# Performance work log

Hardware: AMD Instinct MI355X
Metric: run time of the kernel (lower is better)

## Reference

```python
import jax, jax.numpy as jnp
import numpy as np

N_NODES = 100000
N_EDGES = 1000000
NUM_FEATURES = 64
HIDDEN = 64
NUM_GRAPHS = 128


def setup_inputs() -> dict:
    key = jax.random.key(0)
    ks = jax.random.split(key, 12)
    x = jax.random.normal(ks[0], (N_NODES, NUM_FEATURES), dtype=jnp.float32)
    edge_index = jax.random.randint(ks[1], (2, N_EDGES), 0, N_NODES, dtype=jnp.int64)
    edge_weight = jax.random.uniform(ks[2], (N_EDGES,), dtype=jnp.float32)
    batch = jnp.sort(jax.random.randint(ks[3], (N_NODES,), 0, NUM_GRAPHS, dtype=jnp.int64))
    s1 = 1.0 / np.sqrt(NUM_FEATURES)
    s2 = 1.0 / np.sqrt(HIDDEN)
    # GraphConv layer 1: lin_rel (with bias) applied to aggregated msgs, lin_root (no bias)
    w1_rel = jax.random.uniform(ks[4], (HIDDEN, NUM_FEATURES), jnp.float32, -s1, s1)
    b1_rel = jax.random.uniform(ks[5], (HIDDEN,), jnp.float32, -s1, s1)
    w1_root = jax.random.uniform(ks[6], (HIDDEN, NUM_FEATURES), jnp.float32, -s1, s1)
    # GraphConv layer 2
    w2_rel = jax.random.uniform(ks[7], (HIDDEN, HIDDEN), jnp.float32, -s2, s2)
    b2_rel = jax.random.uniform(ks[8], (HIDDEN,), jnp.float32, -s2, s2)
    w2_root = jax.random.uniform(ks[9], (HIDDEN, HIDDEN), jnp.float32, -s2, s2)
    # final Linear(hidden, 1)
    w_lin = jax.random.uniform(ks[10], (1, HIDDEN), jnp.float32, -s2, s2)
    b_lin = jax.random.uniform(ks[11], (1,), jnp.float32, -s2, s2)
    return {
        "x": x, "edge_index": edge_index, "edge_weight": edge_weight, "batch": batch,
        "w1_rel": w1_rel, "b1_rel": b1_rel, "w1_root": w1_root,
        "w2_rel": w2_rel, "b2_rel": b2_rel, "w2_root": w2_root,
        "w_lin": w_lin, "b_lin": b_lin,
    }


def graph_conv(x, edge_index, edge_weight, w_rel, b_rel, w_root):
    # messages: x[src] * e, scatter-add into dst  (gather-scale-scatter)
    src, dst = edge_index[0], edge_index[1]
    msgs = x[src] * edge_weight[:, None]                      # [E, F]
    aggr = jax.ops.segment_sum(msgs, dst, num_segments=x.shape[0])  # [N, F]
    return aggr @ w_rel.T + b_rel + x @ w_root.T


def reference(x, edge_index, edge_weight, batch,
              w1_rel, b1_rel, w1_root, w2_rel, b2_rel, w2_root, w_lin, b_lin):
    h = graph_conv(x, edge_index, edge_weight, w1_rel, b1_rel, w1_root)
    h = jax.nn.relu(h)
    h = graph_conv(h, edge_index, edge_weight, w2_rel, b2_rel, w2_root)
    # global_mean_pool over graph ids
    sums = jax.ops.segment_sum(h, batch, num_segments=NUM_GRAPHS)          # [G, H]
    counts = jax.ops.segment_sum(jnp.ones((h.shape[0],), h.dtype), batch,
                                 num_segments=NUM_GRAPHS)                  # [G]
    pooled = sums / jnp.maximum(counts, 1.0)[:, None]
    # dropout(p=0.5) in eval mode is identity
    return pooled @ w_lin.T + b_lin                                        # [G, 1]
```

## Files before the change

kernel.cpp:

```cpp
#include <hip/hip_runtime.h>
#include <hip/hip_bf16.h>


#define N_NODES 100000
#define N_EDGES 1000000
#define NGRAPHS 128
#define BN 512
#define NBUCK ((N_NODES + BN - 1) / BN)
#define FILL_T 16
#define FILL_TILE (256 * FILL_T)
#define FILL_NB ((N_EDGES + FILL_TILE - 1) / FILL_TILE)

typedef __attribute__((ext_vector_type(8))) short bf16x8;
typedef __attribute__((ext_vector_type(8))) unsigned short u16x8;
typedef __attribute__((ext_vector_type(4))) float f32x4;

__device__ __forceinline__ unsigned short f2bf(float f) {
    unsigned u = __float_as_uint(f);
    unsigned r = (u + 0x7FFFu + ((u >> 16) & 1u)) >> 16;
    return (unsigned short)r;
}
__device__ __forceinline__ float bf2f(unsigned short h) {
    return __uint_as_float(((unsigned)h) << 16);
}

__global__ __launch_bounds__(256) void prep_cvt_kernel(
    const float* __restrict__ x, unsigned short* __restrict__ xh, int n8,
    const float* __restrict__ w1rel, const float* __restrict__ w1root,
    const float* __restrict__ w2rel, const float* __restrict__ w2root,
    const float* __restrict__ wlin, const float* __restrict__ b2rel,
    const float* __restrict__ blin, unsigned short* __restrict__ whirel,
    unsigned short* __restrict__ wlorel, unsigned short* __restrict__ whiroot,
    unsigned short* __restrict__ wloroot, float* __restrict__ u,
    float* __restrict__ v, float* __restrict__ C) {
    int tid = threadIdx.x;
    int i = blockIdx.x * 256 + tid;
    if (i < n8) {
        const float4* xp = (const float4*)x + (size_t)i * 2;
        float4 a = xp[0], b = xp[1];
        u16x8 o;
        o[0] = f2bf(a.x); o[1] = f2bf(a.y); o[2] = f2bf(a.z); o[3] = f2bf(a.w);
        o[4] = f2bf(b.x); o[5] = f2bf(b.y); o[6] = f2bf(b.z); o[7] = f2bf(b.w);
        *((u16x8*)xh + i) = o;
        return;
    }
    for (int k = tid; k < 4096; k += 256) {
        float a = w1rel[k];
        unsigned short hi = f2bf(a);
        whirel[k] = hi;
        wlorel[k] = f2bf(a - bf2f(hi));
        float b = w1root[k];
        unsigned short hb = f2bf(b);
        whiroot[k] = hb;
        wloroot[k] = f2bf(b - bf2f(hb));
    }
    if (tid < 64) {
        float uu = 0.f, vv = 0.f;
        for (int h = 0; h < 64; ++h) {
            float wl = wlin[h];
            uu += wl * w2rel[h * 64 + tid];
            vv += wl * w2root[h * 64 + tid];
        }
        u[tid] = uu;
        v[tid] = vv;
    }
    if (tid == 0) {
        float c = blin[0];
        for (int h = 0; h < 64; ++h) c += wlin[h] * b2rel[h];
        *C = c;
    }
}

__global__ __launch_bounds__(256) void bucket_hist(const int* __restrict__ ei,
                                                   int* __restrict__ bcount,
                                                   int E) {
    __shared__ int lh[NBUCK];
    int tid = threadIdx.x;
    for (int i = tid; i < NBUCK; i += 256) lh[i] = 0;
    __syncthreads();
    for (int e = blockIdx.x * 256 + tid; e < E; e += gridDim.x * 256)
        atomicAdd(&lh[ei[E + e] >> 9], 1);
    __syncthreads();
    for (int i = tid; i < NBUCK; i += 256) {
        int c = lh[i];
        if (c) atomicAdd(&bcount[i], c);
    }
}

__global__ void bucket_scan(const int* __restrict__ bcount,
                            int* __restrict__ boff, int* __restrict__ cursor) {
    __shared__ int s[256];
    int t = threadIdx.x;
    int v = (t < NBUCK) ? bcount[t] : 0;
    s[t] = v;
    __syncthreads();
    for (int off = 1; off < 256; off <<= 1) {
        int x = (t >= off) ? s[t - off] : 0;
        __syncthreads();
        s[t] += x;
        __syncthreads();
    }
    if (t < NBUCK) {
        boff[t] = s[t] - v;
        cursor[t] = s[t] - v;
    }
    if (t == 255) boff[NBUCK] = s[255];
}

__global__ __launch_bounds__(256) void bucket_fill(
    const int* __restrict__ ei, const float* __restrict__ ew,
    int* __restrict__ cursor, int2* __restrict__ ebuf, int E) {
    __shared__ int lh[NBUCK];
    __shared__ int gbase[NBUCK];
    int tid = threadIdx.x;
    for (int i = tid; i < NBUCK; i += 256) lh[i] = 0;
    __syncthreads();
    int base = blockIdx.x * FILL_TILE;
    int2 rec[FILL_T];
    int meta[FILL_T];
#pragma unroll
    for (int i = 0; i < FILL_T; ++i) {
        int e = base + i * 256 + tid;
        meta[i] = -1;
        if (e < E) {
            int src = ei[e];
            int dst = ei[E + e];
            int b = dst >> 9;
            int r = atomicAdd(&lh[b], 1);
            rec[i].x = src | ((dst & (BN - 1)) << 17);
            rec[i].y = __float_as_int(ew[e]);
            meta[i] = (b << 13) | r;
        }
    }
    __syncthreads();
    for (int i = tid; i < NBUCK; i += 256) {
        int c = lh[i];
        gbase[i] = c ? atomicAdd(&cursor[i], c) : 0;
    }
    __syncthreads();
#pragma unroll
    for (int i = 0; i < FILL_T; ++i) {
        if (meta[i] >= 0) {
            int b = meta[i] >> 13;
            int r = meta[i] & 8191;
            ebuf[gbase[b] + r] = rec[i];
        }
    }
}

__global__ __launch_bounds__(512) void csr_build(
    const int* __restrict__ boff, const int2* __restrict__ ebuf,
    const int* __restrict__ batch, int* __restrict__ row_ptr,
    int2* __restrict__ csr, int N) {
    __shared__ int s[BN];
    int b = blockIdx.x;
    int t = threadIdx.x;
    int beg = boff[b], end = boff[b + 1];
    s[t] = 0;
    __syncthreads();
    for (int j = beg + t; j < end; j += 512)
        atomicAdd(&s[(ebuf[j].x >> 17) & (BN - 1)], 1);
    __syncthreads();
    int v = s[t];
    for (int off = 1; off < BN; off <<= 1) {
        int x = (t >= off) ? s[t - off] : 0;
        __syncthreads();
        s[t] += x;
        __syncthreads();
    }
    int excl = s[t] - v;
    int gidx = b * BN + t;
    if (gidx <= N) row_ptr[gidx] = beg + excl;
    __syncthreads();
    s[t] = excl;
    __syncthreads();
    for (int j = beg + t; j < end; j += 512) {
        int2 rec = ebuf[j];
        int dlo = (rec.x >> 17) & (BN - 1);
        int g = batch[b * BN + dlo];
        int r = atomicAdd(&s[dlo], 1);
        int2 o;
        o.x = (rec.x & 0x1FFFF) | (g << 17);
        o.y = rec.y;
        csr[beg + r] = o;
    }
}

__global__ __launch_bounds__(256) void gather_kernel(
    const unsigned short* __restrict__ xh, const int* __restrict__ row_ptr,
    const int2* __restrict__ csr, unsigned short* __restrict__ aggr, int N,
    int chunk) {
    int lane = threadIdx.x & 63;
    int wid = (blockIdx.x * blockDim.x + threadIdx.x) >> 6;
    int g = lane >> 4;
    int c = lane & 15;
    int n0 = wid * chunk;
    int n1 = min(n0 + chunk, N);
    for (int node = n0; node < n1; ++node) {
        int beg = row_ptr[node], end = row_ptr[node + 1];
        float4 acc = {0.f, 0.f, 0.f, 0.f};
        for (int j0 = beg; j0 < end; j0 += 64) {
            int cnt = min(64, end - j0);
            int2 e = {0, 0};
            if (lane < cnt) e = csr[j0 + lane];
            for (int k = 0; k < cnt; k += 4) {
                int myk = k + g;
                int sj = __shfl(e.x, myk) & 0x1FFFF;
                float wj = __int_as_float(__shfl(e.y, myk));
                if (myk < cnt) {
                    ushort4 xv =
                        *(const ushort4*)(xh + (size_t)sj * 64 + c * 4);
                    acc.x += wj * bf2f(xv.x);
                    acc.y += wj * bf2f(xv.y);
                    acc.z += wj * bf2f(xv.z);
                    acc.w += wj * bf2f(xv.w);
                }
            }
        }
#pragma unroll
        for (int off = 16; off < 64; off <<= 1) {
            acc.x += __shfl_xor(acc.x, off);
            acc.y += __shfl_xor(acc.y, off);
            acc.z += __shfl_xor(acc.z, off);
            acc.w += __shfl_xor(acc.w, off);
        }
        if (lane < 16) {
            ushort4 o;
            o.x = f2bf(acc.x);
            o.y = f2bf(acc.y);
            o.z = f2bf(acc.z);
            o.w = f2bf(acc.w);
            *(ushort4*)(aggr + (size_t)node * 64 + c * 4) = o;
        }
    }
}

__global__ __launch_bounds__(256, 2) void dense_kernel(
    const unsigned short* __restrict__ aggr,
    const unsigned short* __restrict__ xh,
    const unsigned short* __restrict__ whirel,
    const unsigned short* __restrict__ wlorel,
    const unsigned short* __restrict__ whiroot,
    const unsigned short* __restrict__ wloroot,
    const float* __restrict__ b1rel, const float* __restrict__ u,
    const float* __restrict__ v, float* __restrict__ p, float* __restrict__ q,
    int N) {
    int lane = threadIdx.x & 63;
    int wave = (blockIdx.x << 2) + (threadIdx.x >> 6);
    int nb = wave * 16;
    if (nb >= N) return;
    int lo4 = lane & 15;
    int quad = lane >> 4;

    f32x4 acc[4];
#pragma unroll
    for (int t = 0; t < 4; ++t) acc[t] = (f32x4){0.f, 0.f, 0.f, 0.f};

    for (int s = 0; s < 2; ++s) {
        bf16x8 Aa = *(const bf16x8*)(aggr + (size_t)(nb + lo4) * 64 + s * 32 +
                                     quad * 8);
        bf16x8 Ax = *(const bf16x8*)(xh + (size_t)(nb + lo4) * 64 + s * 32 +
                                     quad * 8);
#pragma unroll
        for (int t = 0; t < 4; ++t) {
            int off = (t * 16 + lo4) * 64 + s * 32 + quad * 8;
            bf16x8 bhr = *(const bf16x8*)(whirel + off);
            bf16x8 blr = *(const bf16x8*)(wlorel + off);
            bf16x8 bhx = *(const bf16x8*)(whiroot + off);
            bf16x8 blx = *(const bf16x8*)(wloroot + off);
            acc[t] = __builtin_amdgcn_mfma_f32_16x16x32_bf16(Aa, bhr, acc[t],
                                                             0, 0, 0);
            acc[t] = __builtin_amdgcn_mfma_f32_16x16x32_bf16(Aa, blr, acc[t],
                                                             0, 0, 0);
            acc[t] = __builtin_amdgcn_mfma_f32_16x16x32_bf16(Ax, bhx, acc[t],
                                                             0, 0, 0);
            acc[t] = __builtin_amdgcn_mfma_f32_16x16x32_bf16(Ax, blx, acc[t],
                                                             0, 0, 0);
        }
    }

    float pc[4] = {0.f, 0.f, 0.f, 0.f};
    float qc[4] = {0.f, 0.f, 0.f, 0.f};
#pragma unroll
    for (int t = 0; t < 4; ++t) {
        float bb = b1rel[t * 16 + lo4];
        float uu = u[t * 16 + lo4];
        float vv = v[t * 16 + lo4];
#pragma unroll
        for (int r = 0; r < 4; ++r) {
            float h1 = fmaxf(acc[t][r] + bb, 0.f);
            pc[r] += uu * h1;
            qc[r] += vv * h1;
        }
    }
#pragma unroll
    for (int off = 1; off < 16; off <<= 1) {
#pragma unroll
        for (int r = 0; r < 4; ++r) {
            pc[r] += __shfl_xor(pc[r], off);
            qc[r] += __shfl_xor(qc[r], off);
        }
    }
    if (lo4 == 0) {
        f32x4 po = {pc[0], pc[1], pc[2], pc[3]};
        f32x4 qo = {qc[0], qc[1], qc[2], qc[3]};
        *(f32x4*)(p + nb + quad * 4) = po;
        *(f32x4*)(q + nb + quad * 4) = qo;
    }
}

#define PT_EPT 4
#define PT_EPW (64 * PT_EPT)
#define PT_NB ((N_EDGES + 4 * PT_EPW - 1) / (4 * PT_EPW))
#define PS_NB 98
__global__ __launch_bounds__(256) void pool_both(
    const int2* __restrict__ csr, const float* __restrict__ p,
    const float* __restrict__ q, const int* __restrict__ batch,
    float* __restrict__ gp, float* __restrict__ gq, float* __restrict__ gc,
    int E, int N) {
    __shared__ float lbuf[2 * NGRAPHS];
    int tid = threadIdx.x;
    lbuf[tid] = 0.f;
    __syncthreads();
    if (blockIdx.x < PT_NB) {
        int lane = tid & 63;
        int wid = (blockIdx.x * 256 + tid) >> 6;
        int base = wid * PT_EPW;
        float acc = 0.f;
        int curg = -1;
#pragma unroll
        for (int i = 0; i < PT_EPT; ++i) {
            int j = base + i * 64 + lane;
            if (j < E) {
                int2 e = csr[j];
                int g = (e.x >> 17) & 127;
                float val = __int_as_float(e.y) * p[e.x & 0x1FFFF];
                if (g != curg) {
                    if (curg >= 0) atomicAdd(&lbuf[curg], acc);
                    curg = g;
                    acc = 0.f;
                }
                acc += val;
            }
        }
        if (curg >= 0) atomicAdd(&lbuf[curg], acc);
        __syncthreads();
        if (tid < NGRAPHS) {
            float t = lbuf[tid];
            if (t != 0.f) atomicAdd(&gp[tid], t);
        }
    } else {
        int bid = blockIdx.x - PT_NB;
        for (int i = bid * 256 + tid; i < N; i += PS_NB * 256) {
            int g = batch[i];
            atomicAdd(&lbuf[g], q[i]);
            atomicAdd(&lbuf[NGRAPHS + g], 1.f);
        }
        __syncthreads();
        if (tid < NGRAPHS) {
            if (lbuf[NGRAPHS + tid] != 0.f) {
                atomicAdd(&gq[tid], lbuf[tid]);
                atomicAdd(&gc[tid], lbuf[NGRAPHS + tid]);
            }
        }
    }
}

__global__ void final_kernel(const float* __restrict__ gp,
                             const float* __restrict__ gq,
                             const float* __restrict__ gc,
                             const float* __restrict__ C,
                             float* __restrict__ out) {
    int g = threadIdx.x;
    float c = fmaxf(gc[g], 1.0f);
    out[g] = (gp[g] + gq[g]) / c + *C;
}

extern "C" void kernel_launch(void* const* d_in, const int* in_sizes, int n_in,
                              void* d_out, int out_size, void* d_ws,
                              size_t ws_size, hipStream_t stream) {
    const float* x      = (const float*)d_in[0];
    const int*   ei     = (const int*)d_in[1];
    const float* ew     = (const float*)d_in[2];
    const int*   batch  = (const int*)d_in[3];
    const float* w1rel  = (const float*)d_in[4];
    const float* b1rel  = (const float*)d_in[5];
    const float* w1root = (const float*)d_in[6];
    const float* w2rel  = (const float*)d_in[7];
    const float* b2rel  = (const float*)d_in[8];
    const float* w2root = (const float*)d_in[9];
    const float* wlin   = (const float*)d_in[10];
    const float* blin   = (const float*)d_in[11];
    float* out = (float*)d_out;

    char* wsb = (char*)d_ws;
    int2* csr  = (int2*)wsb;
    unsigned short* aggr = (unsigned short*)(wsb + (size_t)N_EDGES * 8);
    int2* ebuf = (int2*)aggr;
    char* tail = wsb + (size_t)N_EDGES * 8 + (size_t)N_NODES * 128;
    unsigned short* whirel  = (unsigned short*)tail;
    unsigned short* wlorel  = whirel + 4096;
    unsigned short* whiroot = wlorel + 4096;
    unsigned short* wloroot = whiroot + 4096;
    float* p  = (float*)(wloroot + 4096);
    float* q  = p + N_NODES;
    float* u  = q + N_NODES;
    float* v  = u + 64;
    float* C  = v + 64;
    int*   bcount = (int*)(C + 1);
    float* gp = (float*)(bcount + NBUCK);
    float* gq = gp + NGRAPHS;
    float* gc = gq + NGRAPHS;
    int*   boff   = (int*)(gc + NGRAPHS);
    int*   cursor = boff + (NBUCK + 1);
    int*   row_ptr = cursor + NBUCK;
    unsigned short* xh = (unsigned short*)(row_ptr + N_NODES + 2);

    hipMemsetAsync(bcount, 0, (NBUCK + 3 * NGRAPHS) * sizeof(int), stream);

    int n8 = N_NODES * 64 / 8;
    prep_cvt_kernel<<<n8 / 256 + 1, 256, 0, stream>>>(
        x, xh, n8, w1rel, w1root, w2rel, w2root, wlin, b2rel, blin, whirel,
        wlorel, whiroot, wloroot, u, v, C);

    bucket_hist<<<256, 256, 0, stream>>>(ei, bcount, N_EDGES);
    bucket_scan<<<1, 256, 0, stream>>>(bcount, boff, cursor);
    bucket_fill<<<FILL_NB, 256, 0, stream>>>(ei, ew, cursor, ebuf, N_EDGES);
    csr_build<<<NBUCK, 512, 0, stream>>>(boff, ebuf, batch, row_ptr, csr,
                                         N_NODES);

    {
        int blocks = 2048;
        int waves = blocks * 4;
        int chunk = (N_NODES + waves - 1) / waves;
        gather_kernel<<<blocks, 256, 0, stream>>>(xh, row_ptr, csr, aggr,
                                                  N_NODES, chunk);
    }
    {
        int tiles = N_NODES / 16;
        int blocks = (tiles + 3) / 4;
        dense_kernel<<<blocks, 256, 0, stream>>>(aggr, xh, whirel, wlorel,
                                                 whiroot, wloroot, b1rel, u, v,
                                                 p, q, N_NODES);
    }
    pool_both<<<PT_NB + PS_NB, 256, 0, stream>>>(csr, p, q, batch, gp, gq, gc,
                                                 N_EDGES, N_NODES);
    final_kernel<<<1, NGRAPHS, 0, stream>>>(gp, gq, gc, C, out);
}
```

Baseline: 229.7 us.

## Fuse bf16 conversion with bucket histogram; widen gather loads to 16 bytes

Merges the x-to-bf16 conversion, weight prep and edge-destination histogram into one launch, using block-index ranges so the independent jobs run side by side and one kernel launch is saved. The gather kernel now has each lane load 8 bf16 values (16 bytes) instead of 4, so 8 edges are in flight per step rather than 4 and each step issues fewer, wider memory requests. It also doubles the edges handled per thread in the pooling kernel. The risks are more registers per lane in gather, an extra shuffle-reduction stage, and the histogram blocks now competing with the conversion blocks for the GPU at the same time.

```diff
diff --git a/kernel.cpp b/kernel.cpp
--- a/kernel.cpp
+++ b/kernel.cpp
@@ -10,6 +10,8 @@
 #define FILL_T 16
 #define FILL_TILE (256 * FILL_T)
 #define FILL_NB ((N_EDGES + FILL_TILE - 1) / FILL_TILE)
+#define CVT_NB (N_NODES * 64 / 8 / 256)
+#define HIST_NB 256
 
 typedef __attribute__((ext_vector_type(8))) short bf16x8;
 typedef __attribute__((ext_vector_type(8))) unsigned short u16x8;
@@ -24,8 +26,9 @@
     return __uint_as_float(((unsigned)h) << 16);
 }
 
-__global__ __launch_bounds__(256) void prep_cvt_kernel(
-    const float* __restrict__ x, unsigned short* __restrict__ xh, int n8,
+__global__ __launch_bounds__(256) void prep_cvt_hist_kernel(
+    const float* __restrict__ x, unsigned short* __restrict__ xh,
+    const int* __restrict__ ei, int* __restrict__ bcount,
     const float* __restrict__ w1rel, const float* __restrict__ w1root,
     const float* __restrict__ w2rel, const float* __restrict__ w2root,
     const float* __restrict__ wlin, const float* __restrict__ b2rel,
@@ -34,52 +37,51 @@
     unsigned short* __restrict__ wloroot, float* __restrict__ u,
     float* __restrict__ v, float* __restrict__ C) {
     int tid = threadIdx.x;
-    int i = blockIdx.x * 256 + tid;
-    if (i < n8) {
+    int b = blockIdx.x;
+    if (b < CVT_NB) {
+        int i = b * 256 + tid;
         const float4* xp = (const float4*)x + (size_t)i * 2;
-        float4 a = xp[0], b = xp[1];
+        float4 a = xp[0], bb = xp[1];
         u16x8 o;
         o[0] = f2bf(a.x); o[1] = f2bf(a.y); o[2] = f2bf(a.z); o[3] = f2bf(a.w);
-        o[4] = f2bf(b.x); o[5] = f2bf(b.y); o[6] = f2bf(b.z); o[7] = f2bf(b.w);
+        o[4] = f2bf(bb.x); o[5] = f2bf(bb.y); o[6] = f2bf(bb.z); o[7] = f2bf(bb.w);
         *((u16x8*)xh + i) = o;
         return;
     }
-    for (int k = tid; k < 4096; k += 256) {
-        float a = w1rel[k];
-        unsigned short hi = f2bf(a);
-        whirel[k] = hi;
-        wlorel[k] = f2bf(a - bf2f(hi));
-        float b = w1root[k];
-        unsigned short hb = f2bf(b);
-        whiroot[k] = hb;
-        wloroot[k] = f2bf(b - bf2f(hb));
-    }
-    if (tid < 64) {
-        float uu = 0.f, vv = 0.f;
-        for (int h = 0; h < 64; ++h) {
-            float wl = wlin[h];
-            uu += wl * w2rel[h * 64 + tid];
-            vv += wl * w2root[h * 64 + tid];
-        }
-        u[tid] = uu;
-        v[tid] = vv;
-    }
-    if (tid == 0) {
-        float c = blin[0];
-        for (int h = 0; h < 64; ++h) c += wlin[h] * b2rel[h];
-        *C = c;
-    }
-}
-
-__global__ __launch_bounds__(256) void bucket_hist(const int* __restrict__ ei,
-                                                   int* __restrict__ bcount,
-                                                   int E) {
+    if (b == CVT_NB) {
+        for (int k = tid; k < 4096; k += 256) {
+            float a = w1rel[k];
+            unsigned short hi = f2bf(a);
+            whirel[k] = hi;
+            wlorel[k] = f2bf(a - bf2f(hi));
+            float w = w1root[k];
+            unsigned short hb = f2bf(w);
+            whiroot[k] = hb;
+            wloroot[k] = f2bf(w - bf2f(hb));
+        }
+        if (tid < 64) {
+            float uu = 0.f, vv = 0.f;
+            for (int h = 0; h < 64; ++h) {
+                float wl = wlin[h];
+                uu += wl * w2rel[h * 64 + tid];
+                vv += wl * w2root[h * 64 + tid];
+            }
+            u[tid] = uu;
+            v[tid] = vv;
+        }
+        if (tid == 0) {
+            float c = blin[0];
+            for (int h = 0; h < 64; ++h) c += wlin[h] * b2rel[h];
+            *C = c;
+        }
+        return;
+    }
     __shared__ int lh[NBUCK];
-    int tid = threadIdx.x;
+    int hb = b - CVT_NB - 1;
     for (int i = tid; i < NBUCK; i += 256) lh[i] = 0;
     __syncthreads();
-    for (int e = blockIdx.x * 256 + tid; e < E; e += gridDim.x * 256)
-        atomicAdd(&lh[ei[E + e] >> 9], 1);
+    for (int e = hb * 256 + tid; e < N_EDGES; e += HIST_NB * 256)
+        atomicAdd(&lh[ei[N_EDGES + e] >> 9], 1);
     __syncthreads();
     for (int i = tid; i < NBUCK; i += 256) {
         int c = lh[i];
@@ -192,45 +194,40 @@
     int chunk) {
     int lane = threadIdx.x & 63;
     int wid = (blockIdx.x * blockDim.x + threadIdx.x) >> 6;
-    int g = lane >> 4;
-    int c = lane & 15;
+    int g = lane >> 3;
+    int c = lane & 7;
     int n0 = wid * chunk;
     int n1 = min(n0 + chunk, N);
     for (int node = n0; node < n1; ++node) {
         int beg = row_ptr[node], end = row_ptr[node + 1];
-        float4 acc = {0.f, 0.f, 0.f, 0.f};
+        float acc[8];
+#pragma unroll
+        for (int t = 0; t < 8; ++t) acc[t] = 0.f;
         for (int j0 = beg; j0 < end; j0 += 64) {
             int cnt = min(64, end - j0);
             int2 e = {0, 0};
             if (lane < cnt) e = csr[j0 + lane];
-            for (int k = 0; k < cnt; k += 4) {
+            for (int k = 0; k < cnt; k += 8) {
                 int myk = k + g;
                 int sj = __shfl(e.x, myk) & 0x1FFFF;
                 float wj = __int_as_float(__shfl(e.y, myk));
                 if (myk < cnt) {
-                    ushort4 xv =
-                        *(const ushort4*)(xh + (size_t)sj * 64 + c * 4);
-                    acc.x += wj * bf2f(xv.x);
-                    acc.y += wj * bf2f(xv.y);
-                    acc.z += wj * bf2f(xv.z);
-                    acc.w += wj * bf2f(xv.w);
+                    u16x8 xv = *(const u16x8*)(xh + (size_t)sj * 64 + c * 8);
+#pragma unroll
+                    for (int t = 0; t < 8; ++t) acc[t] += wj * bf2f(xv[t]);
                 }
             }
         }
 #pragma unroll
-        for (int off = 16; off < 64; off <<= 1) {
-            acc.x += __shfl_xor(acc.x, off);
-            acc.y += __shfl_xor(acc.y, off);
-            acc.z += __shfl_xor(acc.z, off);
-            acc.w += __shfl_xor(acc.w, off);
-        }
-        if (lane < 16) {
-            ushort4 o;
-            o.x = f2bf(acc.x);
-            o.y = f2bf(acc.y);
-            o.z = f2bf(acc.z);
-            o.w = f2bf(acc.w);
-            *(ushort4*)(aggr + (size_t)node * 64 + c * 4) = o;
+        for (int off = 8; off < 64; off <<= 1) {
+#pragma unroll
+            for (int t = 0; t < 8; ++t) acc[t] += __shfl_xor(acc[t], off);
+        }
+        if (lane < 8) {
+            u16x8 o;
+#pragma unroll
+            for (int t = 0; t < 8; ++t) o[t] = f2bf(acc[t]);
+            *(u16x8*)(aggr + (size_t)node * 64 + c * 8) = o;
         }
     }
 }
@@ -309,7 +306,7 @@
     }
 }
 
-#define PT_EPT 4
+#define PT_EPT 8
 #define PT_EPW (64 * PT_EPT)
 #define PT_NB ((N_EDGES + 4 * PT_EPW - 1) / (4 * PT_EPW))
 #define PS_NB 98
@@ -418,12 +415,10 @@
 
     hipMemsetAsync(bcount, 0, (NBUCK + 3 * NGRAPHS) * sizeof(int), stream);
 
-    int n8 = N_NODES * 64 / 8;
-    prep_cvt_kernel<<<n8 / 256 + 1, 256, 0, stream>>>(
-        x, xh, n8, w1rel, w1root, w2rel, w2root, wlin, b2rel, blin, whirel,
-        wlorel, whiroot, wloroot, u, v, C);
-
-    bucket_hist<<<256, 256, 0, stream>>>(ei, bcount, N_EDGES);
+    prep_cvt_hist_kernel<<<CVT_NB + 1 + HIST_NB, 256, 0, stream>>>(
+        x, xh, ei, bcount, w1rel, w1root, w2rel, w2root, wlin, b2rel, blin,
+        whirel, wlorel, whiroot, wloroot, u, v, C);
+
     bucket_scan<<<1, 256, 0, stream>>>(bcount, boff, cursor);
     bucket_fill<<<FILL_NB, 256, 0, stream>>>(ei, ew, cursor, ebuf, N_EDGES);
     csr_build<<<NBUCK, 512, 0, stream>>>(boff, ebuf, batch, row_ptr, csr,
```

New measurement: 223.9 us. 1.03x faster.
